# Kernel optimization log

Hardware: AMD Instinct MI355X
Metric: run time of the kernel (lower is better)

Reference implementation:

```python
import jax, jax.numpy as jnp
import numpy as np

STATE_DIM, ACTION_DIM, HIDDEN_DIM, GRU_DIM = 256, 64, 1024, 512
BATCH = 65536
IN_DIM = STATE_DIM + ACTION_DIM


def setup_inputs() -> dict:
    key = jax.random.key(0)
    ks = jax.random.split(key, 12)
    s = lambda k, shp, scale: (jax.random.normal(k, shp, jnp.float32) * scale)
    inp = {
        'state': jax.random.normal(ks[0], (BATCH, STATE_DIM), jnp.float32),
        'action': jax.random.normal(ks[1], (BATCH, ACTION_DIM), jnp.float32),
        'hidden': jax.random.normal(ks[2], (1, BATCH, GRU_DIM), jnp.float32),
        # GRU params, PyTorch layout: rows ordered [reset, update, new]
        'w_ih': s(ks[3], (3 * GRU_DIM, IN_DIM), 0.05),
        'w_hh': s(ks[4], (3 * GRU_DIM, GRU_DIM), 0.05),
        'b_ih': jnp.zeros((3 * GRU_DIM,), jnp.float32),
        'b_hh': jnp.zeros((3 * GRU_DIM,), jnp.float32),
        'w1': s(ks[5], (HIDDEN_DIM, GRU_DIM), 0.05),
        'b1': jnp.zeros((HIDDEN_DIM,), jnp.float32),
        'w2': s(ks[6], (HIDDEN_DIM, HIDDEN_DIM), 0.03),
        'b2': jnp.zeros((HIDDEN_DIM,), jnp.float32),
        'w3': s(ks[7], (1, HIDDEN_DIM), 0.03),
        'b3': jnp.zeros((1,), jnp.float32),
    }
    return inp


def reference(state, action, hidden, w_ih, w_hh, b_ih, b_hh, w1, b1, w2, b2, w3, b3):
    # (state, action) -> concat -> single-step GRU -> fc1 -> relu -> fc2 -> relu -> fc3
    sa = jnp.concatenate([state, action], axis=1)          # [B, IN_DIM]
    h = hidden[0]                                           # [B, G]
    gi = sa @ w_ih.T + b_ih                                 # [B, 3G]
    gh = h @ w_hh.T + b_hh                                  # [B, 3G]
    G = h.shape[1]
    i_r, i_z, i_n = gi[:, :G], gi[:, G:2 * G], gi[:, 2 * G:]
    h_r, h_z, h_n = gh[:, :G], gh[:, G:2 * G], gh[:, 2 * G:]
    r = jax.nn.sigmoid(i_r + h_r)
    z = jax.nn.sigmoid(i_z + h_z)
    n = jnp.tanh(i_n + r * h_n)
    h_new = (1.0 - z) * n + z * h                           # [B, G]
    x = jax.nn.relu(h_new @ w1.T + b1)
    x = jax.nn.relu(x @ w2.T + b2)
    q = x @ w3.T + b3                                       # [B, 1]
    return q, h_new[None]
```

## Files before the change

### kernel.cpp

```cpp
#include <hip/hip_runtime.h>
#include <stdint.h>

#define BATCH 65536
#define KCAT 832

typedef __attribute__((ext_vector_type(8))) short bf16x8;
typedef __attribute__((ext_vector_type(4))) float f32x4;

typedef __attribute__((address_space(3))) void lds_void_t;
typedef __attribute__((address_space(1))) void glob_void_t;

__device__ __forceinline__ void async_copy16(const void* g, void* l) {
  __builtin_amdgcn_global_load_lds((glob_void_t*)(uintptr_t)g,
                                   (lds_void_t*)(uint32_t)(uintptr_t)l, 16, 0, 0);
}

__device__ __forceinline__ float b2f(unsigned short u) {
  union { uint32_t i; float f; } c; c.i = ((uint32_t)u) << 16; return c.f;
}
__device__ __forceinline__ unsigned short f2b(float f) {
  uint32_t x = __float_as_uint(f);
  uint32_t r = (x + 0x7fffu + ((x >> 16) & 1u)) >> 16;
  return (unsigned short)r;
}


__global__ void pack_A(const float* __restrict__ state, const float* __restrict__ action,
                       const float* __restrict__ hidden, unsigned short* __restrict__ Acat) {
  long t = (long)blockIdx.x * 256 + threadIdx.x;
  int seg = (int)(t % 104); long row = t / 104;
  int col = seg * 8;
  const float* src;
  if (col < 256)       src = state  + row * 256 + col;
  else if (col < 320)  src = action + row * 64  + (col - 256);
  else                 src = hidden + row * 512 + (col - 320);
  bf16x8 o;
  #pragma unroll
  for (int j = 0; j < 8; j++) o[j] = (short)f2b(src[j]);
  *(bf16x8*)(Acat + row * (size_t)KCAT + col) = o;
}

__global__ void pack_W(const float* __restrict__ w_ih, const float* __restrict__ w_hh,
                       unsigned short* __restrict__ Wrz, unsigned short* __restrict__ Wn) {
  long t = (long)blockIdx.x * 256 + threadIdx.x;
  int seg = (int)(t % 104); int j = (int)(t / 104);
  int col = seg * 8;
  const float* src = (col < 320) ? (w_ih + (long)j * 320 + col)
                                 : (w_hh + (long)j * 512 + (col - 320));
  unsigned short* dst = (j < 1024) ? (Wrz + (long)j * KCAT + col)
                                   : (Wn + (long)(j - 1024) * KCAT + col);
  bf16x8 o;
  #pragma unroll
  for (int jj = 0; jj < 8; jj++) o[jj] = (short)f2b(src[jj]);
  *(bf16x8*)dst = o;
}

__global__ void pack_w12(const float* __restrict__ w1, const float* __restrict__ w2,
                         const float* __restrict__ b3,
                         unsigned short* __restrict__ w1b, unsigned short* __restrict__ w2b,
                         float* __restrict__ q) {
  long t = (long)blockIdx.x * 256 + threadIdx.x;
  if (t < 65536) {
    const float* s = w1 + t * 8; unsigned short* d = w1b + t * 8;
    bf16x8 o;
    #pragma unroll
    for (int j = 0; j < 8; j++) o[j] = (short)f2b(s[j]);
    *(bf16x8*)d = o;
  } else if (t < 196608) {
    long t2 = t - 65536;
    const float* s = w2 + t2 * 8; unsigned short* d = w2b + t2 * 8;
    bf16x8 o;
    #pragma unroll
    for (int j = 0; j < 8; j++) o[j] = (short)f2b(s[j]);
    *(bf16x8*)d = o;
  } else {
    q[t - 196608] = b3[0];
  }
}


__global__ __launch_bounds__(256, 2) void gru_fused(
    const unsigned short* __restrict__ A,
    const unsigned short* __restrict__ Wrz,
    const unsigned short* __restrict__ Wn,
    const float* __restrict__ b_ih, const float* __restrict__ b_hh,
    float* __restrict__ hnew_f,
    unsigned short* __restrict__ hnew_b)
{
  __shared__ unsigned short Asm[128 * 64];
  __shared__ unsigned short Wsm[3 * 64 * 64];
  const int tid = threadIdx.x;
  const int wave = tid >> 6, lane = tid & 63;
  const int wm = wave >> 1, wn = wave & 1;

  const int bid = blockIdx.x;
  const int xcd = bid & 7;
  const int j = bid >> 3;
  const int bn = j & 7;
  const long bm = (long)xcd * 64 + (j >> 3);

  const int srow = lane >> 3;
  const int scol = (((lane & 7) ^ srow)) * 8;

  f32x4 accR[4][2], accZ[4][2], accI[4][2], accH[4][2];
  #pragma unroll
  for (int i = 0; i < 4; i++)
    #pragma unroll
    for (int t = 0; t < 2; t++) {
      accR[i][t] = (f32x4){0.f,0.f,0.f,0.f}; accZ[i][t] = (f32x4){0.f,0.f,0.f,0.f};
      accI[i][t] = (f32x4){0.f,0.f,0.f,0.f}; accH[i][t] = (f32x4){0.f,0.f,0.f,0.f};
    }

  const unsigned short* Ag  = A   + (bm * 128 + wave * 8 + srow) * (size_t)KCAT + scol;
  const unsigned short* Wrg = Wrz + ((size_t)bn * 64 + wave * 8 + srow) * KCAT + scol;
  const unsigned short* Wzg = Wrz + ((size_t)512 + bn * 64 + wave * 8 + srow) * KCAT + scol;
  const unsigned short* Wng = Wn  + ((size_t)bn * 64 + wave * 8 + srow) * KCAT + scol;

  const int rlo = lane & 15;
  const int quad = lane >> 4;

  for (int kt = 0; kt < 13; ++kt) {
    __syncthreads();
    #pragma unroll
    for (int t = 0; t < 4; ++t)
      async_copy16(Ag + (size_t)(t * 32) * KCAT + kt * 64, &Asm[(t * 32 + wave * 8) * 64]);
    #pragma unroll
    for (int t = 0; t < 2; ++t) {
      async_copy16(Wrg + (size_t)(t * 32) * KCAT + kt * 64, &Wsm[0 * 4096 + (t * 32 + wave * 8) * 64]);
      async_copy16(Wzg + (size_t)(t * 32) * KCAT + kt * 64, &Wsm[1 * 4096 + (t * 32 + wave * 8) * 64]);
      async_copy16(Wng + (size_t)(t * 32) * KCAT + kt * 64, &Wsm[2 * 4096 + (t * 32 + wave * 8) * 64]);
    }
    __syncthreads();

    #pragma unroll
    for (int ks = 0; ks < 2; ++ks) {
      const int kseg = ks * 4 + quad;
      const int sw = (kseg ^ (rlo & 7)) * 8;
      bf16x8 af[4], bR[2], bZ[2], bN[2];
      #pragma unroll
      for (int mt = 0; mt < 4; mt++)
        af[mt] = *(const bf16x8*)&Asm[(wm * 64 + mt * 16 + rlo) * 64 + sw];
      #pragma unroll
      for (int nt = 0; nt < 2; nt++) {
        const int wrow = (wn * 32 + nt * 16 + rlo) * 64 + sw;
        bR[nt] = *(const bf16x8*)&Wsm[0 * 4096 + wrow];
        bZ[nt] = *(const bf16x8*)&Wsm[1 * 4096 + wrow];
        bN[nt] = *(const bf16x8*)&Wsm[2 * 4096 + wrow];
      }
      #pragma unroll
      for (int mt = 0; mt < 4; mt++)
        #pragma unroll
        for (int nt = 0; nt < 2; nt++) {
          accR[mt][nt] = __builtin_amdgcn_mfma_f32_16x16x32_bf16(af[mt], bR[nt], accR[mt][nt], 0, 0, 0);
          accZ[mt][nt] = __builtin_amdgcn_mfma_f32_16x16x32_bf16(af[mt], bZ[nt], accZ[mt][nt], 0, 0, 0);
        }
      if (kt < 5) {
        #pragma unroll
        for (int mt = 0; mt < 4; mt++)
          #pragma unroll
          for (int nt = 0; nt < 2; nt++)
            accI[mt][nt] = __builtin_amdgcn_mfma_f32_16x16x32_bf16(af[mt], bN[nt], accI[mt][nt], 0, 0, 0);
      } else {
        #pragma unroll
        for (int mt = 0; mt < 4; mt++)
          #pragma unroll
          for (int nt = 0; nt < 2; nt++)
            accH[mt][nt] = __builtin_amdgcn_mfma_f32_16x16x32_bf16(af[mt], bN[nt], accH[mt][nt], 0, 0, 0);
      }
    }
  }

  const long rowbase = bm * 128 + wm * 64;
  const int colbase = bn * 64 + wn * 32;
  #pragma unroll
  for (int mt = 0; mt < 4; mt++) {
    #pragma unroll
    for (int nt = 0; nt < 2; nt++) {
      const int col = colbase + nt * 16 + rlo;
      const float brv = b_ih[col] + b_hh[col];
      const float bzv = b_ih[512 + col] + b_hh[512 + col];
      const float bin = b_ih[1024 + col];
      const float bhn = b_hh[1024 + col];
      #pragma unroll
      for (int i = 0; i < 4; i++) {
        const long row = rowbase + mt * 16 + quad * 4 + i;
        const float r = 1.f / (1.f + __expf(-(accR[mt][nt][i] + brv)));
        const float z = 1.f / (1.f + __expf(-(accZ[mt][nt][i] + bzv)));
        const float x = (accI[mt][nt][i] + bin) + r * (accH[mt][nt][i] + bhn);
        const float n = 1.f - 2.f / (__expf(2.f * x) + 1.f);
        const float h = b2f(A[row * (size_t)KCAT + 320 + col]);
        const float hv = (1.f - z) * n + z * h;
        hnew_f[row * (size_t)512 + col] = hv;
        hnew_b[row * (size_t)512 + col] = f2b(hv);
      }
    }
  }
}


template<int KT, int QFUSE>
__global__ __launch_bounds__(256, 2) void gemm_bt(
    const unsigned short* __restrict__ A, const unsigned short* __restrict__ W,
    const float* __restrict__ bias, unsigned short* __restrict__ out,
    int lda, const float* __restrict__ w3, float* __restrict__ q)
{
  __shared__ unsigned short Asm[128 * 64];
  __shared__ unsigned short Bsm[128 * 64];
  const int tid = threadIdx.x;
  const int wave = tid >> 6, lane = tid & 63;
  const int wm = wave >> 1, wn = wave & 1;

  const int bid = blockIdx.x;
  const int xcd = bid & 7;
  const int j = bid >> 3;
  const int bn = j & 7;
  const long bm = (long)xcd * 64 + (j >> 3);

  const int srow = lane >> 3;
  const int scol = (((lane & 7) ^ srow)) * 8;

  f32x4 acc[4][4];
  #pragma unroll
  for (int i = 0; i < 4; i++)
    #pragma unroll
    for (int t = 0; t < 4; t++) acc[i][t] = (f32x4){0.f, 0.f, 0.f, 0.f};

  const unsigned short* Ag = A + (bm * 128 + wave * 8 + srow) * (size_t)lda + scol;
  const unsigned short* Wg = W + ((size_t)bn * 128 + wave * 8 + srow) * lda + scol;

  const int rlo = lane & 15;
  const int quad = lane >> 4;

  for (int kt = 0; kt < KT; ++kt) {
    __syncthreads();
    #pragma unroll
    for (int t = 0; t < 4; ++t)
      async_copy16(Ag + (size_t)(t * 32) * lda + kt * 64, &Asm[(t * 32 + wave * 8) * 64]);
    #pragma unroll
    for (int t = 0; t < 4; ++t)
      async_copy16(Wg + (size_t)(t * 32) * lda + kt * 64, &Bsm[(t * 32 + wave * 8) * 64]);
    __syncthreads();

    #pragma unroll
    for (int ks = 0; ks < 2; ++ks) {
      const int kseg = ks * 4 + quad;
      const int sw = (kseg ^ (rlo & 7)) * 8;
      bf16x8 af[4], bfv[4];
      #pragma unroll
      for (int mt = 0; mt < 4; mt++)
        af[mt] = *(const bf16x8*)&Asm[(wm * 64 + mt * 16 + rlo) * 64 + sw];
      #pragma unroll
      for (int nt = 0; nt < 4; nt++)
        bfv[nt] = *(const bf16x8*)&Bsm[(wn * 64 + nt * 16 + rlo) * 64 + sw];
      #pragma unroll
      for (int mt = 0; mt < 4; mt++)
        #pragma unroll
        for (int nt = 0; nt < 4; nt++)
          acc[mt][nt] = __builtin_amdgcn_mfma_f32_16x16x32_bf16(af[mt], bfv[nt], acc[mt][nt], 0, 0, 0);
    }
  }

  if (QFUSE == 0) {
    #pragma unroll
    for (int mt = 0; mt < 4; mt++) {
      #pragma unroll
      for (int nt = 0; nt < 4; nt++) {
        const int col = bn * 128 + wn * 64 + nt * 16 + rlo;
        const float bv = bias[col];
        #pragma unroll
        for (int i = 0; i < 4; i++) {
          const long row = bm * 128 + wm * 64 + mt * 16 + quad * 4 + i;
          float v = fmaxf(acc[mt][nt][i] + bv, 0.f);
          out[row * (size_t)1024 + col] = f2b(v);
        }
      }
    }
  } else {
    float bv[4], w3v[4];
    #pragma unroll
    for (int nt = 0; nt < 4; nt++) {
      const int col = bn * 128 + wn * 64 + nt * 16 + rlo;
      bv[nt] = bias[col];
      w3v[nt] = w3[col];
    }
    #pragma unroll
    for (int mt = 0; mt < 4; mt++) {
      #pragma unroll
      for (int i = 0; i < 4; i++) {
        float s = 0.f;
        #pragma unroll
        for (int nt = 0; nt < 4; nt++)
          s += fmaxf(acc[mt][nt][i] + bv[nt], 0.f) * w3v[nt];
        #pragma unroll
        for (int off = 1; off < 16; off <<= 1) s += __shfl_xor(s, off, 64);
        if (rlo == 0) {
          const long row = bm * 128 + wm * 64 + mt * 16 + quad * 4 + i;
          atomicAdd(&q[row], s);
        }
      }
    }
  }
}


extern "C" void kernel_launch(void* const* d_in, const int* in_sizes, int n_in,
                              void* d_out, int out_size, void* d_ws, size_t ws_size,
                              hipStream_t stream) {
  const float* state  = (const float*)d_in[0];
  const float* action = (const float*)d_in[1];
  const float* hidden = (const float*)d_in[2];
  const float* w_ih   = (const float*)d_in[3];
  const float* w_hh   = (const float*)d_in[4];
  const float* b_ih   = (const float*)d_in[5];
  const float* b_hh   = (const float*)d_in[6];
  const float* w1     = (const float*)d_in[7];
  const float* b1     = (const float*)d_in[8];
  const float* w2     = (const float*)d_in[9];
  const float* b2     = (const float*)d_in[10];
  const float* w3     = (const float*)d_in[11];
  const float* b3     = (const float*)d_in[12];

  float* q_out = (float*)d_out;
  float* h_out = q_out + BATCH;

  char* ws = (char*)d_ws;
  unsigned short* Acat = (unsigned short*)(ws + 0);
  unsigned short* x1   = (unsigned short*)(ws + 0);
  unsigned short* hnb  = (unsigned short*)(ws + 268435456);
  unsigned short* Wrz  = (unsigned short*)(ws + 335544320);
  unsigned short* Wn   = (unsigned short*)(ws + 337248256);
  unsigned short* w1b  = (unsigned short*)(ws + 338100224);
  unsigned short* w2b  = (unsigned short*)(ws + 339148800);

  pack_A<<<26624, 256, 0, stream>>>(state, action, hidden, Acat);
  pack_W<<<624, 256, 0, stream>>>(w_ih, w_hh, Wrz, Wn);
  pack_w12<<<1024, 256, 0, stream>>>(w1, w2, b3, w1b, w2b, q_out);

  gru_fused<<<4096, 256, 0, stream>>>(Acat, Wrz, Wn, b_ih, b_hh, h_out, hnb);
  gemm_bt<8, 0><<<4096, 256, 0, stream>>>(hnb, w1b, b1, x1, 512, nullptr, nullptr);
  gemm_bt<16, 1><<<4096, 256, 0, stream>>>(x1, w2b, b2, nullptr, 1024, w3, q_out);
}
```

Before: 749.8 us.

## Double-buffer LDS tiles to prefetch next K-slice during MFMA compute

Both the fused GRU kernel and the MLP GEMM kernel now keep two LDS buffers for the A and weight tiles. The async global-to-LDS copies for k-tile kt+1 are issued before computing on tile kt, with one barrier per iteration instead of two. This is meant to hide global load latency behind the MFMA work. The cost is double the LDS per block (80 KB for the GRU kernel), which risks occupancy limits at two blocks per CU. It also relies on the barrier waiting for the outstanding async copies.

```diff
diff --git a/kernel.cpp b/kernel.cpp
--- a/kernel.cpp
+++ b/kernel.cpp
@@ -87,8 +87,8 @@
     float* __restrict__ hnew_f,
     unsigned short* __restrict__ hnew_b)
 {
-  __shared__ unsigned short Asm[128 * 64];
-  __shared__ unsigned short Wsm[3 * 64 * 64];
+  __shared__ unsigned short Asm[2][128 * 64];
+  __shared__ unsigned short Wsm[2][3 * 4096];
   const int tid = threadIdx.x;
   const int wave = tid >> 6, lane = tid & 63;
   const int wm = wave >> 1, wn = wave & 1;
@@ -119,18 +119,24 @@
   const int rlo = lane & 15;
   const int quad = lane >> 4;
 
+  auto issue = [&](int kt, int b) {
+    #pragma unroll
+    for (int t = 0; t < 4; ++t)
+      async_copy16(Ag + (size_t)(t * 32) * KCAT + kt * 64, &Asm[b][(t * 32 + wave * 8) * 64]);
+    #pragma unroll
+    for (int t = 0; t < 2; ++t) {
+      async_copy16(Wrg + (size_t)(t * 32) * KCAT + kt * 64, &Wsm[b][0 * 4096 + (t * 32 + wave * 8) * 64]);
+      async_copy16(Wzg + (size_t)(t * 32) * KCAT + kt * 64, &Wsm[b][1 * 4096 + (t * 32 + wave * 8) * 64]);
+      async_copy16(Wng + (size_t)(t * 32) * KCAT + kt * 64, &Wsm[b][2 * 4096 + (t * 32 + wave * 8) * 64]);
+    }
+  };
+
+  issue(0, 0);
+  __syncthreads();
+
   for (int kt = 0; kt < 13; ++kt) {
-    __syncthreads();
-    #pragma unroll
-    for (int t = 0; t < 4; ++t)
-      async_copy16(Ag + (size_t)(t * 32) * KCAT + kt * 64, &Asm[(t * 32 + wave * 8) * 64]);
-    #pragma unroll
-    for (int t = 0; t < 2; ++t) {
-      async_copy16(Wrg + (size_t)(t * 32) * KCAT + kt * 64, &Wsm[0 * 4096 + (t * 32 + wave * 8) * 64]);
-      async_copy16(Wzg + (size_t)(t * 32) * KCAT + kt * 64, &Wsm[1 * 4096 + (t * 32 + wave * 8) * 64]);
-      async_copy16(Wng + (size_t)(t * 32) * KCAT + kt * 64, &Wsm[2 * 4096 + (t * 32 + wave * 8) * 64]);
-    }
-    __syncthreads();
+    const int cb = kt & 1;
+    if (kt < 12) issue(kt + 1, (kt + 1) & 1);
 
     #pragma unroll
     for (int ks = 0; ks < 2; ++ks) {
@@ -139,13 +145,13 @@
       bf16x8 af[4], bR[2], bZ[2], bN[2];
       #pragma unroll
       for (int mt = 0; mt < 4; mt++)
-        af[mt] = *(const bf16x8*)&Asm[(wm * 64 + mt * 16 + rlo) * 64 + sw];
+        af[mt] = *(const bf16x8*)&Asm[cb][(wm * 64 + mt * 16 + rlo) * 64 + sw];
       #pragma unroll
       for (int nt = 0; nt < 2; nt++) {
         const int wrow = (wn * 32 + nt * 16 + rlo) * 64 + sw;
-        bR[nt] = *(const bf16x8*)&Wsm[0 * 4096 + wrow];
-        bZ[nt] = *(const bf16x8*)&Wsm[1 * 4096 + wrow];
-        bN[nt] = *(const bf16x8*)&Wsm[2 * 4096 + wrow];
+        bR[nt] = *(const bf16x8*)&Wsm[cb][0 * 4096 + wrow];
+        bZ[nt] = *(const bf16x8*)&Wsm[cb][1 * 4096 + wrow];
+        bN[nt] = *(const bf16x8*)&Wsm[cb][2 * 4096 + wrow];
       }
       #pragma unroll
       for (int mt = 0; mt < 4; mt++)
@@ -168,6 +174,7 @@
             accH[mt][nt] = __builtin_amdgcn_mfma_f32_16x16x32_bf16(af[mt], bN[nt], accH[mt][nt], 0, 0, 0);
       }
     }
+    __syncthreads();
   }
 
   const long rowbase = bm * 128 + wm * 64;
@@ -204,8 +211,8 @@
     const float* __restrict__ bias, unsigned short* __restrict__ out,
     int lda, const float* __restrict__ w3, float* __restrict__ q)
 {
-  __shared__ unsigned short Asm[128 * 64];
-  __shared__ unsigned short Bsm[128 * 64];
+  __shared__ unsigned short Asm[2][128 * 64];
+  __shared__ unsigned short Bsm[2][128 * 64];
   const int tid = threadIdx.x;
   const int wave = tid >> 6, lane = tid & 63;
   const int wm = wave >> 1, wn = wave & 1;
@@ -231,15 +238,21 @@
   const int rlo = lane & 15;
   const int quad = lane >> 4;
 
+  auto issue = [&](int kt, int b) {
+    #pragma unroll
+    for (int t = 0; t < 4; ++t)
+      async_copy16(Ag + (size_t)(t * 32) * lda + kt * 64, &Asm[b][(t * 32 + wave * 8) * 64]);
+    #pragma unroll
+    for (int t = 0; t < 4; ++t)
+      async_copy16(Wg + (size_t)(t * 32) * lda + kt * 64, &Bsm[b][(t * 32 + wave * 8) * 64]);
+  };
+
+  issue(0, 0);
+  __syncthreads();
+
   for (int kt = 0; kt < KT; ++kt) {
-    __syncthreads();
-    #pragma unroll
-    for (int t = 0; t < 4; ++t)
-      async_copy16(Ag + (size_t)(t * 32) * lda + kt * 64, &Asm[(t * 32 + wave * 8) * 64]);
-    #pragma unroll
-    for (int t = 0; t < 4; ++t)
-      async_copy16(Wg + (size_t)(t * 32) * lda + kt * 64, &Bsm[(t * 32 + wave * 8) * 64]);
-    __syncthreads();
+    const int cb = kt & 1;
+    if (kt + 1 < KT) issue(kt + 1, (kt + 1) & 1);
 
     #pragma unroll
     for (int ks = 0; ks < 2; ++ks) {
@@ -248,16 +261,17 @@
       bf16x8 af[4], bfv[4];
       #pragma unroll
       for (int mt = 0; mt < 4; mt++)
-        af[mt] = *(const bf16x8*)&Asm[(wm * 64 + mt * 16 + rlo) * 64 + sw];
+        af[mt] = *(const bf16x8*)&Asm[cb][(wm * 64 + mt * 16 + rlo) * 64 + sw];
       #pragma unroll
       for (int nt = 0; nt < 4; nt++)
-        bfv[nt] = *(const bf16x8*)&Bsm[(wn * 64 + nt * 16 + rlo) * 64 + sw];
+        bfv[nt] = *(const bf16x8*)&Bsm[cb][(wn * 64 + nt * 16 + rlo) * 64 + sw];
       #pragma unroll
       for (int mt = 0; mt < 4; mt++)
         #pragma unroll
         for (int nt = 0; nt < 4; nt++)
           acc[mt][nt] = __builtin_amdgcn_mfma_f32_16x16x32_bf16(af[mt], bfv[nt], acc[mt][nt], 0, 0, 0);
     }
+    __syncthreads();
   }
 
   if (QFUSE == 0) {
```

Result: slower. 867.4 us (+15.7%).
